# Performance work log

Hardware: AMD Instinct MI355X
Metric: run time of the kernel (lower is better)

## Reference

```python
import jax, jax.numpy as jnp
import numpy as np

B, N_EX, N_KC, D_E, D_C, D_H = 32, 1024, 128, 64, 64, 64


def setup_inputs() -> dict:
    key = jax.random.key(0)
    ks = jax.random.split(key, 20)
    return {
        "h": jax.random.normal(ks[0], (B, N_KC, D_H), jnp.float32),
        "ex": jax.random.uniform(ks[1], (B, N_EX), jnp.float32),
        "su": jax.random.uniform(ks[2], (B,), jnp.float32),
        "ex_graph": jax.random.uniform(ks[3], (N_EX, N_KC), jnp.float32),
        "kc_gamma": jax.random.normal(ks[4], (N_KC, N_KC), jnp.float32),
        "W_ex": jax.random.normal(ks[5], (D_E, 2 * N_EX), jnp.float32) * 0.02,
        "W_kc": jax.random.normal(ks[6], (D_C, N_KC), jnp.float32) * 0.05,
        "tgru_wih": jax.random.normal(ks[7], (3 * D_H, D_E), jnp.float32) * 0.05,
        "tgru_whh": jax.random.normal(ks[8], (3 * D_H, D_H), jnp.float32) * 0.05,
        "tgru_bih": jax.random.normal(ks[9], (3 * D_H,), jnp.float32) * 0.05,
        "tgru_bhh": jax.random.normal(ks[10], (3 * D_H,), jnp.float32) * 0.05,
        "fpart_w": jax.random.normal(ks[11], (D_H, D_C + D_H), jnp.float32) * 0.05,
        "fpart_b": jax.random.normal(ks[12], (D_H,), jnp.float32) * 0.05,
        "ulin_w": jax.random.normal(ks[13], (D_H, D_H), jnp.float32) * 0.05,
        "ulin_b": jax.random.normal(ks[14], (D_H,), jnp.float32) * 0.05,
        "ugru_wih": jax.random.normal(ks[15], (3 * D_H, D_H), jnp.float32) * 0.05,
        "ugru_whh": jax.random.normal(ks[16], (3 * D_H, D_H), jnp.float32) * 0.05,
        "ugru_bih": jax.random.normal(ks[17], (3 * D_H,), jnp.float32) * 0.05,
        "ugru_bhh": jax.random.normal(ks[18], (3 * D_H,), jnp.float32) * 0.05,
    }


def _gru_cell(x, h, wih, whh, bih, bhh):
    # torch.nn.GRUCell: gates in order r, z, n
    gi = x @ wih.T + bih
    gh = h @ whh.T + bhh
    ir, iz, inn = jnp.split(gi, 3, axis=-1)
    hr, hz, hn = jnp.split(gh, 3, axis=-1)
    r = jax.nn.sigmoid(ir + hr)
    z = jax.nn.sigmoid(iz + hz)
    n = jnp.tanh(inn + r * hn)
    return (1.0 - z) * n + z * h


def reference(h, ex, su, ex_graph, kc_gamma, W_ex, W_kc,
              tgru_wih, tgru_whh, tgru_bih, tgru_bhh,
              fpart_w, fpart_b, ulin_w, ulin_b,
              ugru_wih, ugru_whh, ugru_bih, ugru_bhh):
    bsz, n_kc, d_h = h.shape
    kc_graph = jax.nn.sigmoid(kc_gamma)  # (n_kc, n_kc)

    # exercise embedding from [ex*su, ex*(1-su)]
    x_id = jnp.concatenate([ex * su[:, None], ex * (1.0 - su)[:, None]], axis=-1)  # (B, 2*n_ex)
    x = x_id @ W_ex.T  # (B, d_e)

    kci = ex @ ex_graph  # (B, n_kc)
    kci_flat = kci.reshape(bsz * n_kc, 1)

    # temporal GRU update, gated by kci
    x_rep = jnp.broadcast_to(x[:, None, :], (bsz, n_kc, x.shape[-1])).reshape(bsz * n_kc, -1)
    h_flat = h.reshape(bsz * n_kc, d_h)
    th = _gru_cell(x_rep, h_flat, tgru_wih, tgru_whh, tgru_bih, tgru_bhh)
    new_h = (1.0 - kci_flat) * h_flat + kci_flat * th  # (B*n_kc, d_h)

    delta_h = (new_h - h_flat).reshape(bsz, n_kc, d_h)

    # kc_embeddings(eye(n_kc)) == W_kc.T : (n_kc, d_c)
    e = W_kc.T
    # fpart(concat([delta_h_i, e_j])) split into the two weight blocks
    W_dh = fpart_w[:, :d_h]   # acts on delta_h
    W_e = fpart_w[:, d_h:]    # acts on e
    dpart = delta_h @ W_dh.T                      # (B, n_kc_i, d_h)
    epart = e @ W_e.T + fpart_b                   # (n_kc_j, d_h)
    pre = dpart[:, :, None, :] + epart[None, None, :, :]  # (B, i, j, d_h)
    partij = jax.nn.relu(pre)
    partij = partij * kc_graph[None, :, :, None] * kci[:, :, None, None]
    partj = jnp.sum(partij, axis=1)               # (B, n_kc_j, d_h)

    outj = jax.nn.relu(partj @ ulin_w.T + ulin_b).reshape(bsz * n_kc, d_h)
    kcj = (kci @ kc_graph).reshape(bsz * n_kc, 1)

    uh = _gru_cell(outj, new_h, ugru_wih, ugru_whh, ugru_bih, ugru_bhh)
    h_out = (1.0 - kcj) * new_h + kcj * uh
    return h_out.reshape(bsz, n_kc, d_h)
```

## Files before the change

kernel.cpp:

```cpp
#include <hip/hip_runtime.h>
#include <math.h>

#define NB  32
#define NKC 128
#define DH  64
#define NEX 1024
#define G3  192

#define XOFF    0
#define KCIOFF  2048
#define NHOFF   6144
#define DPOFF   268288

__device__ __forceinline__ float sigf(float x) { return 1.0f / (1.0f + expf(-x)); }

__global__ __launch_bounds__(256) void k0_x(
    const float* __restrict__ ex, const float* __restrict__ su,
    const float* __restrict__ W_ex, float* __restrict__ ws)
{
    int t = threadIdx.x, wave = t >> 6, lane = t & 63;
    int b = blockIdx.x >> 3;
    int dbase = (blockIdx.x & 7) * 8;
    float sub = su[b];
    const float* exb = ex + (size_t)b * NEX;
    float er[16];
    #pragma unroll
    for (int i = 0; i < 16; ++i) er[i] = exb[lane + i * 64];
    #pragma unroll
    for (int p = 0; p < 2; ++p) {
        int d = dbase + wave * 2 + p;
        const float* wr = W_ex + (size_t)d * (2 * NEX);
        float a1 = 0.f, a2 = 0.f;
        #pragma unroll
        for (int i = 0; i < 16; ++i) {
            int k = lane + i * 64;
            a1 = fmaf(er[i], wr[k], a1);
            a2 = fmaf(er[i], wr[NEX + k], a2);
        }
        float v = sub * a1 + (1.0f - sub) * a2;
        #pragma unroll
        for (int off = 32; off; off >>= 1) v += __shfl_down(v, off, 64);
        if (lane == 0) ws[XOFF + b * DH + d] = v;
    }
}

__global__ __launch_bounds__(512) void k1_tgru(
    const float* __restrict__ h, const float* __restrict__ ex,
    const float* __restrict__ ex_graph,
    const float* __restrict__ tgru_wih, const float* __restrict__ tgru_whh,
    const float* __restrict__ tgru_bih, const float* __restrict__ tgru_bhh,
    const float* __restrict__ fpart_w, float* __restrict__ ws)
{
    int t = threadIdx.x, wave = t >> 6, lane = t & 63;
    int b = blockIdx.x >> 3;
    int i0 = (blockIdx.x & 7) * 16;

    __shared__ float whhT[32 * 193];
    __shared__ float wihT[32 * 193];
    __shared__ float ht[16 * DH];
    __shared__ float dlt[16 * DH];
    __shared__ float kred[512];
    __shared__ float xs[DH];
    __shared__ float gis[G3];
    __shared__ float bhh3[G3];
    __shared__ float kciL[16];

    {
        int i = t & 15, ks = t >> 4, kb = ks * 32;
        const float* exb = ex + (size_t)b * NEX;
        const float* eg = ex_graph + i0 + i;
        float a = 0.f;
        #pragma unroll 4
        for (int k = 0; k < 32; ++k)
            a = fmaf(exb[kb + k], eg[(size_t)(kb + k) * NKC], a);
        kred[t] = a;
    }
    const float* hb = h + (size_t)(b * NKC + i0) * DH;
    for (int idx = t; idx < 16 * DH; idx += 512) ht[idx] = hb[idx];
    if (t < DH) xs[t] = ws[XOFF + b * DH + t];
    if (t < G3) bhh3[t] = tgru_bhh[t];
    __syncthreads();
    if (t < 16) {
        float s = 0.f;
        #pragma unroll
        for (int r = 0; r < 32; ++r) s += kred[r * 16 + t];
        kciL[t] = s;
        ws[KCIOFF + b * NKC + i0 + t] = s;
    }

    float giA = (t < G3) ? tgru_bih[t] : 0.f;
    float ar[2], az[2], an[2];
    #pragma unroll
    for (int m = 0; m < 2; ++m) {
        ar[m] = bhh3[lane]; az[m] = bhh3[64 + lane]; an[m] = bhh3[128 + lane];
    }
    for (int ch = 0; ch < 2; ++ch) {
        __syncthreads();
        for (int idx = t; idx < G3 * 32; idx += 512) {
            int row = idx >> 5, kk = idx & 31;
            whhT[kk * 193 + row] = tgru_whh[row * DH + ch * 32 + kk];
            wihT[kk * 193 + row] = tgru_wih[row * DH + ch * 32 + kk];
        }
        __syncthreads();
        if (t < G3) {
            for (int kk = 0; kk < 32; ++kk)
                giA = fmaf(wihT[kk * 193 + t], xs[ch * 32 + kk], giA);
        }
        for (int kk = 0; kk < 32; ++kk) {
            float wr = whhT[kk * 193 + lane];
            float wz = whhT[kk * 193 + 64 + lane];
            float wn = whhT[kk * 193 + 128 + lane];
            int k = ch * 32 + kk;
            #pragma unroll
            for (int m = 0; m < 2; ++m) {
                float hk = ht[(wave * 2 + m) * DH + k];
                ar[m] = fmaf(wr, hk, ar[m]);
                az[m] = fmaf(wz, hk, az[m]);
                an[m] = fmaf(wn, hk, an[m]);
            }
        }
    }
    if (t < G3) gis[t] = giA;
    __syncthreads();
    #pragma unroll
    for (int m = 0; m < 2; ++m) {
        int il = wave * 2 + m;
        float hval = ht[il * DH + lane];
        float r = sigf(gis[lane] + ar[m]);
        float z = sigf(gis[64 + lane] + az[m]);
        float n = tanhf(gis[128 + lane] + r * an[m]);
        float th = (1.0f - z) * n + z * hval;
        float kv = kciL[il];
        float nh = (1.0f - kv) * hval + kv * th;
        ws[NHOFF + (size_t)(b * NKC + i0 + il) * DH + lane] = nh;
        dlt[il * DH + lane] = kv * (th - hval);
    }
    __syncthreads();
    for (int idx = t; idx < 4096; idx += 512) {
        int d = idx >> 6, k = idx & 63;
        whhT[k * 65 + d] = fpart_w[d * 128 + k];
    }
    __syncthreads();
    float acc[2] = {0.f, 0.f};
    for (int k = 0; k < 64; ++k) {
        float w = whhT[k * 65 + lane];
        #pragma unroll
        for (int m = 0; m < 2; ++m)
            acc[m] = fmaf(dlt[(wave * 2 + m) * DH + k], w, acc[m]);
    }
    #pragma unroll
    for (int m = 0; m < 2; ++m)
        ws[DPOFF + (size_t)(b * NKC + i0 + wave * 2 + m) * DH + lane] = acc[m];
}

__global__ __launch_bounds__(512) void kB_update(
    const float* __restrict__ kc_gamma, const float* __restrict__ W_kc,
    const float* __restrict__ fpart_w, const float* __restrict__ fpart_b,
    const float* __restrict__ ulin_w, const float* __restrict__ ulin_b,
    const float* __restrict__ ugru_wih, const float* __restrict__ ugru_whh,
    const float* __restrict__ ugru_bih, const float* __restrict__ ugru_bhh,
    float* __restrict__ ws, float* __restrict__ out)
{
    int t = threadIdx.x, wave = t >> 6, lane = t & 63;
    int b = blockIdx.x >> 3;
    int j0 = (blockIdx.x & 7) * 16;

    __shared__ float scratch[12352];
    __shared__ float wkS[64 * 17];
    __shared__ float epS[1024];
    __shared__ float pjS[1024];
    __shared__ float outjS[1024];
    __shared__ float newhS[1024];
    __shared__ float kciF[NKC];
    __shared__ float kcjS[16];
    __shared__ float bihS[G3];
    __shared__ float bhhS[G3];

    float* dpartS = scratch;
    float* fwT    = scratch + 8192;

    const float* dp = ws + DPOFF + (size_t)b * NKC * DH;
    for (int idx = t; idx < NKC * DH; idx += 512) dpartS[idx] = dp[idx];
    for (int idx = t; idx < 4096; idx += 512) {
        int d = idx >> 6, c = idx & 63;
        fwT[c * 65 + d] = fpart_w[d * 128 + 64 + c];
    }
    for (int idx = t; idx < 1024; idx += 512) {
        int c = idx >> 4, jl = idx & 15;
        wkS[c * 17 + jl] = W_kc[(size_t)c * NKC + j0 + jl];
        newhS[idx] = ws[NHOFF + (size_t)(b * NKC + j0) * DH + idx];
    }
    if (t < NKC) kciF[t] = ws[KCIOFF + b * NKC + t];
    if (t < G3) { bihS[t] = ugru_bih[t]; bhhS[t] = ugru_bhh[t]; }
    __syncthreads();
    #pragma unroll
    for (int r = 0; r < 2; ++r) {
        int idx = t + r * 512;
        int jl = idx >> 6, d = idx & 63;
        float a = fpart_b[d];
        for (int c = 0; c < 64; ++c)
            a = fmaf(wkS[c * 17 + jl], fwT[c * 65 + d], a);
        epS[jl * DH + d] = a;
    }
    __syncthreads();
    float* wjS = scratch + 8192;
    for (int idx = t; idx < 2048; idx += 512) {
        int i = idx >> 4, jl = idx & 15;
        wjS[idx] = kciF[i] * sigf(kc_gamma[i * NKC + j0 + jl]);
    }
    __syncthreads();
    if (t < 16) {
        float s = 0.f;
        for (int i = 0; i < NKC; ++i) s += wjS[i * 16 + t];
        kcjS[t] = s;
    }
    float ep[2], pa[2];
    #pragma unroll
    for (int m = 0; m < 2; ++m) {
        ep[m] = epS[(wave * 2 + m) * DH + lane]; pa[m] = 0.f;
    }
    for (int i = 0; i < NKC; ++i) {
        float dv = dpartS[i * DH + lane];
        #pragma unroll
        for (int m = 0; m < 2; ++m) {
            float pre = fmaxf(dv + ep[m], 0.f);
            pa[m] = fmaf(pre, wjS[i * 16 + wave * 2 + m], pa[m]);
        }
    }
    #pragma unroll
    for (int m = 0; m < 2; ++m) pjS[(wave * 2 + m) * DH + lane] = pa[m];
    __syncthreads();
    float* ulT = scratch;
    for (int idx = t; idx < 4096; idx += 512) {
        int d2 = idx >> 6, k = idx & 63;
        ulT[k * 65 + d2] = ulin_w[d2 * DH + k];
    }
    float ulb = ulin_b[lane];
    __syncthreads();
    #pragma unroll
    for (int m = 0; m < 2; ++m) {
        int jl = wave * 2 + m;
        float a = ulb;
        for (int k = 0; k < DH; ++k)
            a = fmaf(pjS[jl * DH + k], ulT[k * 65 + lane], a);
        outjS[jl * DH + lane] = fmaxf(a, 0.f);
    }
    float* wihT = scratch;
    float* whhT = scratch + 6176;
    float gir[2], giz[2], gin[2], ghr[2], ghz[2], ghn[2];
    #pragma unroll
    for (int m = 0; m < 2; ++m)
        gir[m] = giz[m] = gin[m] = ghr[m] = ghz[m] = ghn[m] = 0.f;
    for (int ch = 0; ch < 2; ++ch) {
        __syncthreads();
        for (int idx = t; idx < G3 * 32; idx += 512) {
            int row = idx >> 5, kk = idx & 31;
            wihT[kk * 193 + row] = ugru_wih[row * DH + ch * 32 + kk];
            whhT[kk * 193 + row] = ugru_whh[row * DH + ch * 32 + kk];
        }
        __syncthreads();
        for (int kk = 0; kk < 32; ++kk) {
            float wir = wihT[kk * 193 + lane];
            float wiz = wihT[kk * 193 + 64 + lane];
            float win = wihT[kk * 193 + 128 + lane];
            float wwr = whhT[kk * 193 + lane];
            float wwz = whhT[kk * 193 + 64 + lane];
            float wwn = whhT[kk * 193 + 128 + lane];
            int k = ch * 32 + kk;
            #pragma unroll
            for (int m = 0; m < 2; ++m) {
                int jl = wave * 2 + m;
                float ov = outjS[jl * DH + k];
                float nv = newhS[jl * DH + k];
                gir[m] = fmaf(wir, ov, gir[m]);
                giz[m] = fmaf(wiz, ov, giz[m]);
                gin[m] = fmaf(win, ov, gin[m]);
                ghr[m] = fmaf(wwr, nv, ghr[m]);
                ghz[m] = fmaf(wwz, nv, ghz[m]);
                ghn[m] = fmaf(wwn, nv, ghn[m]);
            }
        }
    }
    #pragma unroll
    for (int m = 0; m < 2; ++m) {
        int jl = wave * 2 + m;
        float r = sigf(gir[m] + bihS[lane] + ghr[m] + bhhS[lane]);
        float z = sigf(giz[m] + bihS[64 + lane] + ghz[m] + bhhS[64 + lane]);
        float n = tanhf(gin[m] + bihS[128 + lane] + r * (ghn[m] + bhhS[128 + lane]));
        float nh = newhS[jl * DH + lane];
        float uh = (1.0f - z) * n + z * nh;
        float kj = kcjS[jl];
        out[(size_t)(b * NKC + j0 + jl) * DH + lane] = (1.0f - kj) * nh + kj * uh;
    }
}

extern "C" void kernel_launch(void* const* d_in, const int* in_sizes, int n_in,
                              void* d_out, int out_size, void* d_ws, size_t ws_size,
                              hipStream_t stream) {
    const float* h        = (const float*)d_in[0];
    const float* ex       = (const float*)d_in[1];
    const float* su       = (const float*)d_in[2];
    const float* ex_graph = (const float*)d_in[3];
    const float* kc_gamma = (const float*)d_in[4];
    const float* W_ex     = (const float*)d_in[5];
    const float* W_kc     = (const float*)d_in[6];
    const float* tgru_wih = (const float*)d_in[7];
    const float* tgru_whh = (const float*)d_in[8];
    const float* tgru_bih = (const float*)d_in[9];
    const float* tgru_bhh = (const float*)d_in[10];
    const float* fpart_w  = (const float*)d_in[11];
    const float* fpart_b  = (const float*)d_in[12];
    const float* ulin_w   = (const float*)d_in[13];
    const float* ulin_b   = (const float*)d_in[14];
    const float* ugru_wih = (const float*)d_in[15];
    const float* ugru_whh = (const float*)d_in[16];
    const float* ugru_bih = (const float*)d_in[17];
    const float* ugru_bhh = (const float*)d_in[18];
    float* ws  = (float*)d_ws;
    float* out = (float*)d_out;

    hipLaunchKernelGGL(k0_x, dim3(256), dim3(256), 0, stream,
                       ex, su, W_ex, ws);
    hipLaunchKernelGGL(k1_tgru, dim3(256), dim3(512), 0, stream,
                       h, ex, ex_graph, tgru_wih, tgru_whh, tgru_bih,
                       tgru_bhh, fpart_w, ws);
    hipLaunchKernelGGL(kB_update, dim3(256), dim3(512), 0, stream,
                       kc_gamma, W_kc, fpart_w, fpart_b, ulin_w, ulin_b,
                       ugru_wih, ugru_whh, ugru_bih, ugru_bhh, ws, out);
}
```

Baseline: 137.9 us.

## Vectorize LDS weight staging and matvec loops with padded row-major float4 layouts

Replaces the transposed scalar shared-memory weight layouts (stride 193/65) with row-major layouts padded to 36/68/132 floats, so global-to-LDS copies and inner dot products use float4 loads. The dpart intermediate is now written transposed (d-major) to the workspace so the update kernel can read it with float4 along i, and the kc_graph weights are stored j-major. This aims to cut LDS instruction count and global load transactions, at the cost of a larger scratch buffer, an extra shared transpose plus barriers in the first kernel, and possible bank conflicts from the per-lane row-strided float4 reads.

Result: faster. 127.0 us (median of 2 runs) (-7.9%).

```diff
diff --git a/kernel.cpp b/kernel.cpp
--- a/kernel.cpp
+++ b/kernel.cpp
@@ -13,6 +13,9 @@
 #define DPOFF   268288
 
 __device__ __forceinline__ float sigf(float x) { return 1.0f / (1.0f + expf(-x)); }
+__device__ __forceinline__ float dot4(float4 a, float4 b) {
+    return fmaf(a.x, b.x, fmaf(a.y, b.y, fmaf(a.z, b.z, a.w * b.w)));
+}
 
 __global__ __launch_bounds__(256) void k0_x(
     const float* __restrict__ ex, const float* __restrict__ su,
@@ -55,12 +58,12 @@
     int b = blockIdx.x >> 3;
     int i0 = (blockIdx.x & 7) * 16;
 
-    __shared__ float whhT[32 * 193];
-    __shared__ float wihT[32 * 193];
-    __shared__ float ht[16 * DH];
-    __shared__ float dlt[16 * DH];
+    __shared__ __align__(16) float whh68[G3 * 36];
+    __shared__ __align__(16) float wih68[G3 * 36];
+    __shared__ __align__(16) float ht[16 * DH];
+    __shared__ __align__(16) float dlt[16 * DH];
+    __shared__ __align__(16) float xs[DH];
     __shared__ float kred[512];
-    __shared__ float xs[DH];
     __shared__ float gis[G3];
     __shared__ float bhh3[G3];
     __shared__ float kciL[16];
@@ -96,27 +99,34 @@
     }
     for (int ch = 0; ch < 2; ++ch) {
         __syncthreads();
-        for (int idx = t; idx < G3 * 32; idx += 512) {
-            int row = idx >> 5, kk = idx & 31;
-            whhT[kk * 193 + row] = tgru_whh[row * DH + ch * 32 + kk];
-            wihT[kk * 193 + row] = tgru_wih[row * DH + ch * 32 + kk];
+        for (int idx = t; idx < G3 * 8; idx += 512) {
+            int row = idx >> 3, q = idx & 7;
+            *(float4*)&whh68[row * 36 + 4 * q] =
+                *(const float4*)&tgru_whh[row * DH + ch * 32 + 4 * q];
+            *(float4*)&wih68[row * 36 + 4 * q] =
+                *(const float4*)&tgru_wih[row * DH + ch * 32 + 4 * q];
         }
         __syncthreads();
         if (t < G3) {
-            for (int kk = 0; kk < 32; ++kk)
-                giA = fmaf(wihT[kk * 193 + t], xs[ch * 32 + kk], giA);
-        }
-        for (int kk = 0; kk < 32; ++kk) {
-            float wr = whhT[kk * 193 + lane];
-            float wz = whhT[kk * 193 + 64 + lane];
-            float wn = whhT[kk * 193 + 128 + lane];
-            int k = ch * 32 + kk;
+            #pragma unroll
+            for (int q = 0; q < 8; ++q) {
+                float4 wv = *(float4*)&wih68[t * 36 + 4 * q];
+                float4 xv = *(float4*)&xs[ch * 32 + 4 * q];
+                giA += dot4(wv, xv);
+            }
+        }
+        #pragma unroll
+        for (int q = 0; q < 8; ++q) {
+            float4 wr = *(float4*)&whh68[lane * 36 + 4 * q];
+            float4 wz = *(float4*)&whh68[(64 + lane) * 36 + 4 * q];
+            float4 wn = *(float4*)&whh68[(128 + lane) * 36 + 4 * q];
+            int kb = ch * 32 + 4 * q;
             #pragma unroll
             for (int m = 0; m < 2; ++m) {
-                float hk = ht[(wave * 2 + m) * DH + k];
-                ar[m] = fmaf(wr, hk, ar[m]);
-                az[m] = fmaf(wz, hk, az[m]);
-                an[m] = fmaf(wn, hk, an[m]);
+                float4 hk = *(float4*)&ht[(wave * 2 + m) * DH + kb];
+                ar[m] += dot4(wr, hk);
+                az[m] += dot4(wz, hk);
+                an[m] += dot4(wn, hk);
             }
         }
     }
@@ -136,21 +146,31 @@
         dlt[il * DH + lane] = kv * (th - hval);
     }
     __syncthreads();
-    for (int idx = t; idx < 4096; idx += 512) {
-        int d = idx >> 6, k = idx & 63;
-        whhT[k * 65 + d] = fpart_w[d * 128 + k];
+    float* fw68 = whh68;
+    for (int idx = t; idx < 64 * 16; idx += 512) {
+        int d = idx >> 4, q = idx & 15;
+        *(float4*)&fw68[d * 68 + 4 * q] = *(const float4*)&fpart_w[d * 128 + 4 * q];
     }
     __syncthreads();
     float acc[2] = {0.f, 0.f};
-    for (int k = 0; k < 64; ++k) {
-        float w = whhT[k * 65 + lane];
-        #pragma unroll
-        for (int m = 0; m < 2; ++m)
-            acc[m] = fmaf(dlt[(wave * 2 + m) * DH + k], w, acc[m]);
-    }
-    #pragma unroll
-    for (int m = 0; m < 2; ++m)
-        ws[DPOFF + (size_t)(b * NKC + i0 + wave * 2 + m) * DH + lane] = acc[m];
+    #pragma unroll
+    for (int q = 0; q < 16; ++q) {
+        float4 w = *(float4*)&fw68[lane * 68 + 4 * q];
+        #pragma unroll
+        for (int m = 0; m < 2; ++m) {
+            float4 dv = *(float4*)&dlt[(wave * 2 + m) * DH + 4 * q];
+            acc[m] += dot4(w, dv);
+        }
+    }
+    float* dptT = wih68;
+    __syncthreads();
+    #pragma unroll
+    for (int m = 0; m < 2; ++m) dptT[lane * 17 + wave * 2 + m] = acc[m];
+    __syncthreads();
+    for (int idx = t; idx < 1024; idx += 512) {
+        int d = idx >> 4, il = idx & 15;
+        ws[DPOFF + (size_t)b * 8192 + d * NKC + i0 + il] = dptT[d * 17 + il];
+    }
 }
 
 __global__ __launch_bounds__(512) void kB_update(
@@ -165,30 +185,39 @@
     int b = blockIdx.x >> 3;
     int j0 = (blockIdx.x & 7) * 16;
 
-    __shared__ float scratch[12352];
-    __shared__ float wkS[64 * 17];
-    __shared__ float epS[1024];
-    __shared__ float pjS[1024];
-    __shared__ float outjS[1024];
-    __shared__ float newhS[1024];
+    __shared__ __align__(16) float scratch[13888];
+    __shared__ __align__(16) float pjS[1024];
+    __shared__ __align__(16) float outjS[1024];
+    __shared__ __align__(16) float newhS[1024];
+    __shared__ __align__(16) float epS[1024];
     __shared__ float kciF[NKC];
     __shared__ float kcjS[16];
     __shared__ float bihS[G3];
     __shared__ float bhhS[G3];
 
-    float* dpartS = scratch;
-    float* fwT    = scratch + 8192;
-
-    const float* dp = ws + DPOFF + (size_t)b * NKC * DH;
-    for (int idx = t; idx < NKC * DH; idx += 512) dpartS[idx] = dp[idx];
-    for (int idx = t; idx < 4096; idx += 512) {
-        int d = idx >> 6, c = idx & 63;
-        fwT[c * 65 + d] = fpart_w[d * 128 + 64 + c];
+    float* dpT  = scratch;
+    float* fw68 = scratch + 8448;
+    float* wkT  = scratch + 12800;
+
+    const float* dp = ws + DPOFF + (size_t)b * 8192;
+    #pragma unroll
+    for (int r = 0; r < 4; ++r) {
+        int idx4 = t + r * 512;
+        int d = idx4 >> 5, qi = idx4 & 31;
+        *(float4*)&dpT[d * 132 + 4 * qi] = *(const float4*)&dp[d * NKC + 4 * qi];
+    }
+    for (int idx = t; idx < 64 * 16; idx += 512) {
+        int d = idx >> 4, q = idx & 15;
+        *(float4*)&fw68[d * 68 + 4 * q] =
+            *(const float4*)&fpart_w[d * 128 + 64 + 4 * q];
     }
     for (int idx = t; idx < 1024; idx += 512) {
         int c = idx >> 4, jl = idx & 15;
-        wkS[c * 17 + jl] = W_kc[(size_t)c * NKC + j0 + jl];
-        newhS[idx] = ws[NHOFF + (size_t)(b * NKC + j0) * DH + idx];
+        wkT[jl * 68 + c] = W_kc[(size_t)c * NKC + j0 + jl];
+    }
+    if (t < 256) {
+        const float* nhp = ws + NHOFF + (size_t)(b * NKC + j0) * DH;
+        *(float4*)&newhS[t * 4] = *(const float4*)&nhp[t * 4];
     }
     if (t < NKC) kciF[t] = ws[KCIOFF + b * NKC + t];
     if (t < G3) { bihS[t] = ugru_bih[t]; bhhS[t] = ugru_bhh[t]; }
@@ -198,20 +227,28 @@
         int idx = t + r * 512;
         int jl = idx >> 6, d = idx & 63;
         float a = fpart_b[d];
-        for (int c = 0; c < 64; ++c)
-            a = fmaf(wkS[c * 17 + jl], fwT[c * 65 + d], a);
+        #pragma unroll
+        for (int q = 0; q < 16; ++q) {
+            float4 fv = *(float4*)&fw68[d * 68 + 4 * q];
+            float4 wv = *(float4*)&wkT[jl * 68 + 4 * q];
+            a += dot4(fv, wv);
+        }
         epS[jl * DH + d] = a;
     }
     __syncthreads();
-    float* wjS = scratch + 8192;
+    float* wjT = scratch + 8448;
     for (int idx = t; idx < 2048; idx += 512) {
         int i = idx >> 4, jl = idx & 15;
-        wjS[idx] = kciF[i] * sigf(kc_gamma[i * NKC + j0 + jl]);
+        wjT[jl * 132 + i] = kciF[i] * sigf(kc_gamma[i * NKC + j0 + jl]);
     }
     __syncthreads();
     if (t < 16) {
         float s = 0.f;
-        for (int i = 0; i < NKC; ++i) s += wjS[i * 16 + t];
+        #pragma unroll
+        for (int qi = 0; qi < 32; ++qi) {
+            float4 v = *(float4*)&wjT[t * 132 + 4 * qi];
+            s += v.x + v.y + v.z + v.w;
+        }
         kcjS[t] = s;
     }
     float ep[2], pa[2];
@@ -219,65 +256,76 @@
     for (int m = 0; m < 2; ++m) {
         ep[m] = epS[(wave * 2 + m) * DH + lane]; pa[m] = 0.f;
     }
-    for (int i = 0; i < NKC; ++i) {
-        float dv = dpartS[i * DH + lane];
+    for (int qi = 0; qi < 32; ++qi) {
+        float4 dv = *(float4*)&dpT[lane * 132 + 4 * qi];
         #pragma unroll
         for (int m = 0; m < 2; ++m) {
-            float pre = fmaxf(dv + ep[m], 0.f);
-            pa[m] = fmaf(pre, wjS[i * 16 + wave * 2 + m], pa[m]);
+            float4 wv = *(float4*)&wjT[(wave * 2 + m) * 132 + 4 * qi];
+            pa[m] = fmaf(fmaxf(dv.x + ep[m], 0.f), wv.x, pa[m]);
+            pa[m] = fmaf(fmaxf(dv.y + ep[m], 0.f), wv.y, pa[m]);
+            pa[m] = fmaf(fmaxf(dv.z + ep[m], 0.f), wv.z, pa[m]);
+            pa[m] = fmaf(fmaxf(dv.w + ep[m], 0.f), wv.w, pa[m]);
         }
     }
     #pragma unroll
     for (int m = 0; m < 2; ++m) pjS[(wave * 2 + m) * DH + lane] = pa[m];
     __syncthreads();
-    float* ulT = scratch;
-    for (int idx = t; idx < 4096; idx += 512) {
-        int d2 = idx >> 6, k = idx & 63;
-        ulT[k * 65 + d2] = ulin_w[d2 * DH + k];
+    float* ul68 = scratch;
+    for (int idx = t; idx < 64 * 16; idx += 512) {
+        int d = idx >> 4, q = idx & 15;
+        *(float4*)&ul68[d * 68 + 4 * q] = *(const float4*)&ulin_w[d * DH + 4 * q];
     }
     float ulb = ulin_b[lane];
     __syncthreads();
-    #pragma unroll
-    for (int m = 0; m < 2; ++m) {
-        int jl = wave * 2 + m;
-        float a = ulb;
-        for (int k = 0; k < DH; ++k)
-            a = fmaf(pjS[jl * DH + k], ulT[k * 65 + lane], a);
-        outjS[jl * DH + lane] = fmaxf(a, 0.f);
-    }
-    float* wihT = scratch;
-    float* whhT = scratch + 6176;
+    float oa[2] = {ulb, ulb};
+    #pragma unroll
+    for (int q = 0; q < 16; ++q) {
+        float4 uv = *(float4*)&ul68[lane * 68 + 4 * q];
+        #pragma unroll
+        for (int m = 0; m < 2; ++m) {
+            float4 pv = *(float4*)&pjS[(wave * 2 + m) * DH + 4 * q];
+            oa[m] += dot4(uv, pv);
+        }
+    }
+    #pragma unroll
+    for (int m = 0; m < 2; ++m)
+        outjS[(wave * 2 + m) * DH + lane] = fmaxf(oa[m], 0.f);
+    float* wih36 = scratch;
+    float* whh36 = scratch + 6912;
     float gir[2], giz[2], gin[2], ghr[2], ghz[2], ghn[2];
     #pragma unroll
     for (int m = 0; m < 2; ++m)
         gir[m] = giz[m] = gin[m] = ghr[m] = ghz[m] = ghn[m] = 0.f;
     for (int ch = 0; ch < 2; ++ch) {
         __syncthreads();
-        for (int idx = t; idx < G3 * 32; idx += 512) {
-            int row = idx >> 5, kk = idx & 31;
-            wihT[kk * 193 + row] = ugru_wih[row * DH + ch * 32 + kk];
-            whhT[kk * 193 + row] = ugru_whh[row * DH + ch * 32 + kk];
+        for (int idx = t; idx < G3 * 8; idx += 512) {
+            int row = idx >> 3, q = idx & 7;
+            *(float4*)&wih36[row * 36 + 4 * q] =
+                *(const float4*)&ugru_wih[row * DH + ch * 32 + 4 * q];
+            *(float4*)&whh36[row * 36 + 4 * q] =
+                *(const float4*)&ugru_whh[row * DH + ch * 32 + 4 * q];
         }
         __syncthreads();
-        for (int kk = 0; kk < 32; ++kk) {
-            float wir = wihT[kk * 193 + lane];
-            float wiz = wihT[kk * 193 + 64 + lane];
-            float win = wihT[kk * 193 + 128 + lane];
-            float wwr = whhT[kk * 193 + lane];
-            float wwz = whhT[kk * 193 + 64 + lane];
-            float wwn = whhT[kk * 193 + 128 + lane];
-            int k = ch * 32 + kk;
+        #pragma unroll
+        for (int q = 0; q < 8; ++q) {
+            float4 wir = *(float4*)&wih36[lane * 36 + 4 * q];
+            float4 wiz = *(float4*)&wih36[(64 + lane) * 36 + 4 * q];
+            float4 win = *(float4*)&wih36[(128 + lane) * 36 + 4 * q];
+            float4 wwr = *(float4*)&whh36[lane * 36 + 4 * q];
+            float4 wwz = *(float4*)&whh36[(64 + lane) * 36 + 4 * q];
+            float4 wwn = *(float4*)&whh36[(128 + lane) * 36 + 4 * q];
+            int kb = ch * 32 + 4 * q;
             #pragma unroll
             for (int m = 0; m < 2; ++m) {
                 int jl = wave * 2 + m;
-                float ov = outjS[jl * DH + k];
-                float nv = newhS[jl * DH + k];
-                gir[m] = fmaf(wir, ov, gir[m]);
-                giz[m] = fmaf(wiz, ov, giz[m]);
-                gin[m] = fmaf(win, ov, gin[m]);
-                ghr[m] = fmaf(wwr, nv, ghr[m]);
-                ghz[m] = fmaf(wwz, nv, ghz[m]);
-                ghn[m] = fmaf(wwn, nv, ghn[m]);
+                float4 ov = *(float4*)&outjS[jl * DH + kb];
+                float4 nv = *(float4*)&newhS[jl * DH + kb];
+                gir[m] += dot4(wir, ov);
+                giz[m] += dot4(wiz, ov);
+                gin[m] += dot4(win, ov);
+                ghr[m] += dot4(wwr, nv);
+                ghz[m] += dot4(wwz, nv);
+                ghn[m] += dot4(wwn, nv);
             }
         }
     }
```
